# Kernel optimization log

Hardware: AMD Instinct MI355X
Metric: run time of the kernel (lower is better)

Reference implementation:

```python
import jax, jax.numpy as jnp
import numpy as np

B, L, T = 8, 4096, 128
D_H, D_G, D_PROJ = 1024, 256, 256


def setup_inputs() -> dict:
    key = jax.random.key(0)
    k1, k2, k3, k4, k5 = jax.random.split(key, 5)
    H = jax.random.normal(k1, (B, L, D_H), dtype=jnp.float32)
    G = jax.random.normal(k2, (B, T, D_G), dtype=jnp.float32)
    mask = jax.random.randint(k3, (B, L), 0, 2) == 1  # True = masked out
    Wk = jax.random.normal(k4, (D_H, D_PROJ), dtype=jnp.float32) * 0.02
    Wq = jax.random.normal(k5, (D_G, D_PROJ), dtype=jnp.float32) * 0.02
    return {"H": H, "G": G, "mask": mask, "Wk": Wk, "Wq": Wq}


def reference(H, G, mask, Wk, Wq):
    scale = D_PROJ ** (-0.5)
    K = jnp.einsum('bld,dp->blp', H, Wk)          # [B, L, d_proj]
    Q = jnp.einsum('btd,dp->btp', G, Wq)          # [B, T, d_proj]
    logits = jnp.einsum('btp,blp->btl', Q, K) * scale  # [B, T, L]
    logits = jnp.where(mask[:, None, :], -jnp.inf, logits)
    alpha = jax.nn.softmax(logits, axis=-1)       # [B, T, L]
    Z = jnp.einsum('btl,bld->btd', alpha, H)      # [B, T, d_h]
    return Z
```

## Files before the change

kernel.cpp:

```cpp
#include <hip/hip_runtime.h>
#include <hip/hip_bf16.h>
#include <math.h>

#define B_  8
#define L_  4096
#define T_  128
#define DH  1024
#define DG  256
#define DP  256
#define BK  64

typedef short bf16x8 __attribute__((ext_vector_type(8)));
typedef float f32x4  __attribute__((ext_vector_type(4)));

#define AS1(p) ((const __attribute__((address_space(1))) void*)(p))
#define AS3(p) ((__attribute__((address_space(3))) void*)(p))

__device__ __forceinline__ unsigned short f2bf(float f) {
    unsigned u = __float_as_uint(f);
    unsigned r = (u + 0x7FFFu + ((u >> 16) & 1u)) >> 16;
    return (unsigned short)r;
}

__global__ __launch_bounds__(256) void wct_kernel(const float* __restrict__ Wk,
                                                  const float* __restrict__ Wq,
                                                  unsigned short* __restrict__ Wct) {
    __shared__ __attribute__((aligned(16))) unsigned short As[128 * BK];
    __shared__ __attribute__((aligned(16))) unsigned short Bs[64 * BK];
    const int n0 = blockIdx.x * 64, m0 = blockIdx.y * 128;
    const int tid = threadIdx.x, wave = tid >> 6, lane = tid & 63;
    const int lm = lane & 15, quad = lane >> 4;
    const int wm = wave >> 1, wn = wave & 1;
    const int bc = (tid & 15) * 4, br = tid >> 4;
    f32x4 acc[4][2] = {};

    for (int k0 = 0; k0 < DP; k0 += BK) {
        #pragma unroll
        for (int s = 0; s < 8; ++s) {
            const int row = br + s * 16;
            const float4 v = *(const float4*)(Wk + (size_t)(m0 + row) * DP + k0 + bc);
            ushort4 p; p.x = f2bf(v.x); p.y = f2bf(v.y); p.z = f2bf(v.z); p.w = f2bf(v.w);
            *(ushort4*)(&As[row * BK + bc]) = p;
        }
        #pragma unroll
        for (int s = 0; s < 4; ++s) {
            const int row = br + s * 16;
            const float4 v = *(const float4*)(Wq + (size_t)(n0 + row) * DP + k0 + bc);
            ushort4 p; p.x = f2bf(v.x); p.y = f2bf(v.y); p.z = f2bf(v.z); p.w = f2bf(v.w);
            *(ushort4*)(&Bs[row * BK + bc]) = p;
        }
        __syncthreads();
        #pragma unroll
        for (int ks = 0; ks < 2; ++ks) {
            bf16x8 a[4], bf[2];
            #pragma unroll
            for (int i = 0; i < 4; ++i)
                a[i] = *(const bf16x8*)(&As[(wm * 64 + i * 16 + lm) * BK + ks * 32 + quad * 8]);
            #pragma unroll
            for (int j = 0; j < 2; ++j)
                bf[j] = *(const bf16x8*)(&Bs[(wn * 32 + j * 16 + lm) * BK + ks * 32 + quad * 8]);
            #pragma unroll
            for (int i = 0; i < 4; ++i)
                #pragma unroll
                for (int j = 0; j < 2; ++j)
                    acc[i][j] = __builtin_amdgcn_mfma_f32_16x16x32_bf16(a[i], bf[j], acc[i][j], 0, 0, 0);
        }
        __syncthreads();
    }
    unsigned short* Cb = Wct + (size_t)m0 * DG + n0;
    #pragma unroll
    for (int i = 0; i < 4; ++i)
        #pragma unroll
        for (int j = 0; j < 2; ++j)
            #pragma unroll
            for (int r = 0; r < 4; ++r)
                Cb[(size_t)(wm * 64 + i * 16 + quad * 4 + r) * DG + wn * 32 + j * 16 + lm] =
                    f2bf(acc[i][j][r] * 0.0625f);
}

__global__ __launch_bounds__(256) void qproj_kernel(const float* __restrict__ G,
                                                    const unsigned short* __restrict__ Wct,
                                                    unsigned short* __restrict__ Qk) {
    __shared__ __attribute__((aligned(16))) unsigned short As[128 * BK];
    __shared__ __attribute__((aligned(16))) unsigned short Bs[64 * BK];
    const int n0 = blockIdx.x * 64, m0 = blockIdx.y * 128;
    const int tid = threadIdx.x, wave = tid >> 6, lane = tid & 63;
    const int lm = lane & 15, quad = lane >> 4;
    const int wm = wave >> 1, wn = wave & 1;
    const int bc = (tid & 15) * 4, br = tid >> 4;
    const int ar = lane >> 3, akb = (lane & 7) * 8;
    f32x4 acc[4][2] = {};

    for (int k0 = 0; k0 < DG; k0 += BK) {
        #pragma unroll
        for (int s = 0; s < 8; ++s) {
            const int row = br + s * 16;
            const float4 v = *(const float4*)(G + (size_t)(m0 + row) * DG + k0 + bc);
            ushort4 p; p.x = f2bf(v.x); p.y = f2bf(v.y); p.z = f2bf(v.z); p.w = f2bf(v.w);
            *(ushort4*)(&As[row * BK + bc]) = p;
        }
        #pragma unroll
        for (int s = 0; s < 2; ++s) {
            const int rowb = s * 32 + wave * 8;
            const unsigned short* gp = Wct + (size_t)(n0 + rowb + ar) * DG + k0 + akb;
            __builtin_amdgcn_global_load_lds(AS1(gp), AS3(&Bs[rowb * BK]), 16, 0, 0);
        }
        __syncthreads();
        #pragma unroll
        for (int ks = 0; ks < 2; ++ks) {
            bf16x8 a[4], bf[2];
            #pragma unroll
            for (int i = 0; i < 4; ++i)
                a[i] = *(const bf16x8*)(&As[(wm * 64 + i * 16 + lm) * BK + ks * 32 + quad * 8]);
            #pragma unroll
            for (int j = 0; j < 2; ++j)
                bf[j] = *(const bf16x8*)(&Bs[(wn * 32 + j * 16 + lm) * BK + ks * 32 + quad * 8]);
            #pragma unroll
            for (int i = 0; i < 4; ++i)
                #pragma unroll
                for (int j = 0; j < 2; ++j)
                    acc[i][j] = __builtin_amdgcn_mfma_f32_16x16x32_bf16(a[i], bf[j], acc[i][j], 0, 0, 0);
        }
        __syncthreads();
    }
    unsigned short* Cb = Qk + (size_t)m0 * DH + n0;
    #pragma unroll
    for (int i = 0; i < 4; ++i)
        #pragma unroll
        for (int j = 0; j < 2; ++j)
            #pragma unroll
            for (int r = 0; r < 4; ++r)
                Cb[(size_t)(wm * 64 + i * 16 + quad * 4 + r) * DH + wn * 32 + j * 16 + lm] =
                    f2bf(acc[i][j][r]);
}

__global__ __launch_bounds__(256) void logits_kernel(const unsigned short* __restrict__ Qk,
                                                     const float* __restrict__ H,
                                                     float* __restrict__ logits) {
    __shared__ __attribute__((aligned(16))) unsigned short As[T_ * BK];
    __shared__ __attribute__((aligned(16))) unsigned short Bs[64 * BK];
    const int b = blockIdx.y, l0 = blockIdx.x * 64;
    const int tid = threadIdx.x, wave = tid >> 6, lane = tid & 63;
    const unsigned short* Ab = Qk + (size_t)b * T_ * DH;
    const float*          Hb = H + ((size_t)b * L_ + l0) * DH;

    const int lm = lane & 15, quad = lane >> 4;
    const int wm = wave >> 1, wn = wave & 1;
    f32x4 acc[4][2] = {};
    const int ar = lane >> 3, akb = (lane & 7) * 8;
    const int bc = (tid & 15) * 4, br0 = tid >> 4;

    for (int k0 = 0; k0 < DH; k0 += BK) {
        #pragma unroll
        for (int s = 0; s < 4; ++s) {
            const int rowb = s * 32 + wave * 8;
            const unsigned short* gp = Ab + (size_t)(rowb + ar) * DH + k0 + akb;
            __builtin_amdgcn_global_load_lds(AS1(gp), AS3(&As[rowb * BK]), 16, 0, 0);
        }
        #pragma unroll
        for (int s = 0; s < 4; ++s) {
            const int row = br0 + s * 16;
            const float4 v = *(const float4*)(Hb + (size_t)row * DH + k0 + bc);
            ushort4 p; p.x = f2bf(v.x); p.y = f2bf(v.y); p.z = f2bf(v.z); p.w = f2bf(v.w);
            *(ushort4*)(&Bs[row * BK + bc]) = p;
        }
        __syncthreads();
        #pragma unroll
        for (int ks = 0; ks < 2; ++ks) {
            bf16x8 a[4], bf[2];
            #pragma unroll
            for (int i = 0; i < 4; ++i)
                a[i] = *(const bf16x8*)(&As[(wm * 64 + i * 16 + lm) * BK + ks * 32 + quad * 8]);
            #pragma unroll
            for (int j = 0; j < 2; ++j)
                bf[j] = *(const bf16x8*)(&Bs[(wn * 32 + j * 16 + lm) * BK + ks * 32 + quad * 8]);
            #pragma unroll
            for (int i = 0; i < 4; ++i)
                #pragma unroll
                for (int j = 0; j < 2; ++j)
                    acc[i][j] = __builtin_amdgcn_mfma_f32_16x16x32_bf16(a[i], bf[j], acc[i][j], 0, 0, 0);
        }
        __syncthreads();
    }
    float* Cb = logits + (size_t)b * T_ * L_ + l0;
    #pragma unroll
    for (int i = 0; i < 4; ++i)
        #pragma unroll
        for (int j = 0; j < 2; ++j)
            #pragma unroll
            for (int r = 0; r < 4; ++r)
                Cb[(size_t)(wm * 64 + i * 16 + quad * 4 + r) * L_ + wn * 32 + j * 16 + lm] = acc[i][j][r];
}

__global__ __launch_bounds__(256) void softmax_kernel(const float* __restrict__ logits,
                                                      const int* __restrict__ mask,
                                                      unsigned short* __restrict__ alpha) {
    const int row = blockIdx.x;
    const int b   = row >> 7;
    const int tid = threadIdx.x;
    const float4* p4 = (const float4*)(logits + (size_t)row * L_);
    const int4*   m4 = (const int4*)(mask + (size_t)b * L_);

    float vals[4][4];
    float vmax = -3.0e38f;
    #pragma unroll
    for (int s = 0; s < 4; ++s) {
        const int idx = tid + s * 256;
        float4 v = p4[idx];
        const int4 mm = m4[idx];
        v.x = mm.x ? -3.0e38f : v.x;
        v.y = mm.y ? -3.0e38f : v.y;
        v.z = mm.z ? -3.0e38f : v.z;
        v.w = mm.w ? -3.0e38f : v.w;
        vals[s][0] = v.x; vals[s][1] = v.y; vals[s][2] = v.z; vals[s][3] = v.w;
        vmax = fmaxf(vmax, fmaxf(fmaxf(v.x, v.y), fmaxf(v.z, v.w)));
    }
    #pragma unroll
    for (int off = 32; off; off >>= 1) vmax = fmaxf(vmax, __shfl_down(vmax, off, 64));

    __shared__ float red[4];
    __shared__ float bcast;
    const int wid = tid >> 6, lane = tid & 63;
    if (lane == 0) red[wid] = vmax;
    __syncthreads();
    if (tid == 0) bcast = fmaxf(fmaxf(red[0], red[1]), fmaxf(red[2], red[3]));
    __syncthreads();
    const float m = bcast;

    float sum = 0.f;
    #pragma unroll
    for (int s = 0; s < 4; ++s)
        #pragma unroll
        for (int i = 0; i < 4; ++i) {
            vals[s][i] = __expf(vals[s][i] - m);
            sum += vals[s][i];
        }
    #pragma unroll
    for (int off = 32; off; off >>= 1) sum += __shfl_down(sum, off, 64);
    __syncthreads();
    if (lane == 0) red[wid] = sum;
    __syncthreads();
    if (tid == 0) bcast = red[0] + red[1] + red[2] + red[3];
    __syncthreads();
    const float inv = 1.0f / bcast;

    unsigned short* arow = alpha + (size_t)row * L_;
    #pragma unroll
    for (int s = 0; s < 4; ++s) {
        ushort4 p;
        p.x = f2bf(vals[s][0] * inv); p.y = f2bf(vals[s][1] * inv);
        p.z = f2bf(vals[s][2] * inv); p.w = f2bf(vals[s][3] * inv);
        *(ushort4*)(arow + (size_t)(tid + s * 256) * 4) = p;
    }
}

__global__ __launch_bounds__(256) void z_kernel(const unsigned short* __restrict__ alpha,
                                                const float* __restrict__ H,
                                                float* __restrict__ Z) {
    __shared__ __attribute__((aligned(16))) unsigned short As[T_ * BK];
    __shared__ __attribute__((aligned(16))) unsigned short Bs[64 * (BK + 2)];
    const int d0 = blockIdx.x * 64, b = blockIdx.y, ch = blockIdx.z;
    const int tid = threadIdx.x, wave = tid >> 6, lane = tid & 63;
    const int Lc = L_ / 4;
    const unsigned short* Ab = alpha + (size_t)b * T_ * L_ + ch * Lc;
    const float*          Hb = H + ((size_t)b * L_ + ch * Lc) * DH + d0;

    const int lm = lane & 15, quad = lane >> 4;
    const int wm = wave >> 1, wn = wave & 1;
    f32x4 acc[4][2] = {};
    const int ar = lane >> 3, akb = (lane & 7) * 8;
    const int dg = tid & 7, lp = tid >> 3;
    unsigned* B32 = (unsigned*)Bs;

    for (int k0 = 0; k0 < Lc; k0 += BK) {
        #pragma unroll
        for (int s = 0; s < 4; ++s) {
            const int rowb = s * 32 + wave * 8;
            const unsigned short* gp = Ab + (size_t)(rowb + ar) * L_ + k0 + akb;
            __builtin_amdgcn_global_load_lds(AS1(gp), AS3(&As[rowb * BK]), 16, 0, 0);
        }
        {
            const float* r0 = Hb + (size_t)(k0 + 2 * lp) * DH + dg * 8;
            const float4 v0a = *(const float4*)(r0);
            const float4 v0b = *(const float4*)(r0 + 4);
            const float4 v1a = *(const float4*)(r0 + DH);
            const float4 v1b = *(const float4*)(r0 + DH + 4);
            float a0[8] = {v0a.x, v0a.y, v0a.z, v0a.w, v0b.x, v0b.y, v0b.z, v0b.w};
            float a1[8] = {v1a.x, v1a.y, v1a.z, v1a.w, v1b.x, v1b.y, v1b.z, v1b.w};
            #pragma unroll
            for (int i = 0; i < 8; ++i) {
                const int d = dg * 8 + i;
                B32[d * 33 + lp] = (unsigned)f2bf(a0[i]) | ((unsigned)f2bf(a1[i]) << 16);
            }
        }
        __syncthreads();
        #pragma unroll
        for (int ks = 0; ks < 2; ++ks) {
            bf16x8 a[4], bf[2];
            #pragma unroll
            for (int i = 0; i < 4; ++i)
                a[i] = *(const bf16x8*)(&As[(wm * 64 + i * 16 + lm) * BK + ks * 32 + quad * 8]);
            #pragma unroll
            for (int j = 0; j < 2; ++j) {
                const int d = wn * 32 + j * 16 + lm;
                const unsigned* p = B32 + d * 33 + ks * 16 + quad * 4;
                union { bf16x8 v; unsigned u[4]; } f;
                f.u[0] = p[0]; f.u[1] = p[1]; f.u[2] = p[2]; f.u[3] = p[3];
                bf[j] = f.v;
            }
            #pragma unroll
            for (int i = 0; i < 4; ++i)
                #pragma unroll
                for (int j = 0; j < 2; ++j)
                    acc[i][j] = __builtin_amdgcn_mfma_f32_16x16x32_bf16(a[i], bf[j], acc[i][j], 0, 0, 0);
        }
        __syncthreads();
    }
    float* Cb = Z + (size_t)b * T_ * DH + d0;
    #pragma unroll
    for (int i = 0; i < 4; ++i)
        #pragma unroll
        for (int j = 0; j < 2; ++j)
            #pragma unroll
            for (int r = 0; r < 4; ++r)
                atomicAdd(&Cb[(size_t)(wm * 64 + i * 16 + quad * 4 + r) * DH + wn * 32 + j * 16 + lm],
                          acc[i][j][r]);
}

extern "C" void kernel_launch(void* const* d_in, const int* in_sizes, int n_in,
                              void* d_out, int out_size, void* d_ws, size_t ws_size,
                              hipStream_t stream) {
    const float* H    = (const float*)d_in[0];
    const float* G    = (const float*)d_in[1];
    const int*   mask = (const int*)d_in[2];
    const float* Wk   = (const float*)d_in[3];
    const float* Wq   = (const float*)d_in[4];
    float* Z = (float*)d_out;

    char* ws = (char*)d_ws;
    unsigned short* Wct    = (unsigned short*)ws;
    unsigned short* Qk     = (unsigned short*)(ws + ((size_t)1 << 20));
    float*          logits = (float*)(ws + ((size_t)4 << 20));
    unsigned short* alpha  = (unsigned short*)(ws + ((size_t)24 << 20));

    hipMemsetAsync(Z, 0, (size_t)out_size * sizeof(float), stream);
    wct_kernel<<<dim3(DG / 64, DH / 128), 256, 0, stream>>>(Wk, Wq, Wct);
    qproj_kernel<<<dim3(DH / 64, (B_ * T_) / 128), 256, 0, stream>>>(G, Wct, Qk);
    logits_kernel<<<dim3(L_ / 64, B_), 256, 0, stream>>>(Qk, H, logits);
    softmax_kernel<<<B_ * T_, 256, 0, stream>>>(logits, mask, alpha);
    z_kernel<<<dim3(DH / 64, B_, 4), 256, 0, stream>>>(alpha, H, Z);
}
```

Baseline: 285.4 us.

## Widen GEMM tiles to 128, split logits K into two partials, swizzle z LDS

The logits kernel now uses 128-wide L tiles and splits the D_H reduction into two halves. Each half writes a partial logits buffer, and softmax sums the two partials. The z kernel uses 128-wide D tiles, splits L into 8 chunks instead of 4, and adds an XOR-style rotation to the transposed LDS layout to avoid bank conflicts. Larger tiles reuse each Qk/alpha tile more per H load, at the cost of an extra partial logits buffer read/written, more atomics, and higher register pressure (launch_bounds 256,2).

After: 306.1 us. +7.3%, slower.

```diff
diff --git a/kernel.cpp b/kernel.cpp
--- a/kernel.cpp
+++ b/kernel.cpp
@@ -134,23 +134,23 @@
                     f2bf(acc[i][j][r]);
 }
 
-__global__ __launch_bounds__(256) void logits_kernel(const unsigned short* __restrict__ Qk,
-                                                     const float* __restrict__ H,
-                                                     float* __restrict__ logits) {
+__global__ __launch_bounds__(256, 2) void logits_kernel(const unsigned short* __restrict__ Qk,
+                                                        const float* __restrict__ H,
+                                                        float* __restrict__ part) {
     __shared__ __attribute__((aligned(16))) unsigned short As[T_ * BK];
-    __shared__ __attribute__((aligned(16))) unsigned short Bs[64 * BK];
-    const int b = blockIdx.y, l0 = blockIdx.x * 64;
+    __shared__ __attribute__((aligned(16))) unsigned short Bs[128 * BK];
+    const int l0 = blockIdx.x * 128, b = blockIdx.y, h = blockIdx.z;
     const int tid = threadIdx.x, wave = tid >> 6, lane = tid & 63;
-    const unsigned short* Ab = Qk + (size_t)b * T_ * DH;
-    const float*          Hb = H + ((size_t)b * L_ + l0) * DH;
+    const unsigned short* Ab = Qk + (size_t)b * T_ * DH + h * 512;
+    const float*          Hb = H + ((size_t)b * L_ + l0) * DH + h * 512;
 
     const int lm = lane & 15, quad = lane >> 4;
     const int wm = wave >> 1, wn = wave & 1;
-    f32x4 acc[4][2] = {};
+    f32x4 acc[4][4] = {};
     const int ar = lane >> 3, akb = (lane & 7) * 8;
-    const int bc = (tid & 15) * 4, br0 = tid >> 4;
-
-    for (int k0 = 0; k0 < DH; k0 += BK) {
+    const int bc = (tid & 15) * 4, br = tid >> 4;
+
+    for (int k0 = 0; k0 < 512; k0 += BK) {
         #pragma unroll
         for (int s = 0; s < 4; ++s) {
             const int rowb = s * 32 + wave * 8;
@@ -158,8 +158,8 @@
             __builtin_amdgcn_global_load_lds(AS1(gp), AS3(&As[rowb * BK]), 16, 0, 0);
         }
         #pragma unroll
-        for (int s = 0; s < 4; ++s) {
-            const int row = br0 + s * 16;
+        for (int s = 0; s < 8; ++s) {
+            const int row = br + s * 16;
             const float4 v = *(const float4*)(Hb + (size_t)row * DH + k0 + bc);
             ushort4 p; p.x = f2bf(v.x); p.y = f2bf(v.y); p.z = f2bf(v.z); p.w = f2bf(v.w);
             *(ushort4*)(&Bs[row * BK + bc]) = p;
@@ -167,38 +167,39 @@
         __syncthreads();
         #pragma unroll
         for (int ks = 0; ks < 2; ++ks) {
-            bf16x8 a[4], bf[2];
+            bf16x8 a[4], bf[4];
             #pragma unroll
             for (int i = 0; i < 4; ++i)
                 a[i] = *(const bf16x8*)(&As[(wm * 64 + i * 16 + lm) * BK + ks * 32 + quad * 8]);
             #pragma unroll
-            for (int j = 0; j < 2; ++j)
-                bf[j] = *(const bf16x8*)(&Bs[(wn * 32 + j * 16 + lm) * BK + ks * 32 + quad * 8]);
-            #pragma unroll
-            for (int i = 0; i < 4; ++i)
-                #pragma unroll
-                for (int j = 0; j < 2; ++j)
+            for (int j = 0; j < 4; ++j)
+                bf[j] = *(const bf16x8*)(&Bs[(wn * 64 + j * 16 + lm) * BK + ks * 32 + quad * 8]);
+            #pragma unroll
+            for (int i = 0; i < 4; ++i)
+                #pragma unroll
+                for (int j = 0; j < 4; ++j)
                     acc[i][j] = __builtin_amdgcn_mfma_f32_16x16x32_bf16(a[i], bf[j], acc[i][j], 0, 0, 0);
         }
         __syncthreads();
     }
-    float* Cb = logits + (size_t)b * T_ * L_ + l0;
+    float* Cb = part + ((size_t)h * B_ + b) * T_ * L_ + l0;
     #pragma unroll
     for (int i = 0; i < 4; ++i)
         #pragma unroll
-        for (int j = 0; j < 2; ++j)
+        for (int j = 0; j < 4; ++j)
             #pragma unroll
             for (int r = 0; r < 4; ++r)
-                Cb[(size_t)(wm * 64 + i * 16 + quad * 4 + r) * L_ + wn * 32 + j * 16 + lm] = acc[i][j][r];
-}
-
-__global__ __launch_bounds__(256) void softmax_kernel(const float* __restrict__ logits,
+                Cb[(size_t)(wm * 64 + i * 16 + quad * 4 + r) * L_ + wn * 64 + j * 16 + lm] = acc[i][j][r];
+}
+
+__global__ __launch_bounds__(256) void softmax_kernel(const float* __restrict__ part,
                                                       const int* __restrict__ mask,
                                                       unsigned short* __restrict__ alpha) {
     const int row = blockIdx.x;
     const int b   = row >> 7;
     const int tid = threadIdx.x;
-    const float4* p4 = (const float4*)(logits + (size_t)row * L_);
+    const float4* p0 = (const float4*)(part + (size_t)row * L_);
+    const float4* p1 = (const float4*)(part + (size_t)B_ * T_ * L_ + (size_t)row * L_);
     const int4*   m4 = (const int4*)(mask + (size_t)b * L_);
 
     float vals[4][4];
@@ -206,12 +207,13 @@
     #pragma unroll
     for (int s = 0; s < 4; ++s) {
         const int idx = tid + s * 256;
-        float4 v = p4[idx];
+        const float4 a = p0[idx], c = p1[idx];
         const int4 mm = m4[idx];
-        v.x = mm.x ? -3.0e38f : v.x;
-        v.y = mm.y ? -3.0e38f : v.y;
-        v.z = mm.z ? -3.0e38f : v.z;
-        v.w = mm.w ? -3.0e38f : v.w;
+        float4 v;
+        v.x = mm.x ? -3.0e38f : a.x + c.x;
+        v.y = mm.y ? -3.0e38f : a.y + c.y;
+        v.z = mm.z ? -3.0e38f : a.z + c.z;
+        v.w = mm.w ? -3.0e38f : a.w + c.w;
         vals[s][0] = v.x; vals[s][1] = v.y; vals[s][2] = v.z; vals[s][3] = v.w;
         vmax = fmaxf(vmax, fmaxf(fmaxf(v.x, v.y), fmaxf(v.z, v.w)));
     }
@@ -254,23 +256,22 @@
     }
 }
 
-__global__ __launch_bounds__(256) void z_kernel(const unsigned short* __restrict__ alpha,
-                                                const float* __restrict__ H,
-                                                float* __restrict__ Z) {
+__global__ __launch_bounds__(256, 2) void z_kernel(const unsigned short* __restrict__ alpha,
+                                                   const float* __restrict__ H,
+                                                   float* __restrict__ Z) {
     __shared__ __attribute__((aligned(16))) unsigned short As[T_ * BK];
-    __shared__ __attribute__((aligned(16))) unsigned short Bs[64 * (BK + 2)];
-    const int d0 = blockIdx.x * 64, b = blockIdx.y, ch = blockIdx.z;
+    __shared__ __attribute__((aligned(16))) unsigned B32[128 * 33];
+    const int d0 = blockIdx.x * 128, b = blockIdx.y, ch = blockIdx.z;
     const int tid = threadIdx.x, wave = tid >> 6, lane = tid & 63;
-    const int Lc = L_ / 4;
+    const int Lc = 512;
     const unsigned short* Ab = alpha + (size_t)b * T_ * L_ + ch * Lc;
     const float*          Hb = H + ((size_t)b * L_ + ch * Lc) * DH + d0;
 
     const int lm = lane & 15, quad = lane >> 4;
     const int wm = wave >> 1, wn = wave & 1;
-    f32x4 acc[4][2] = {};
+    f32x4 acc[4][4] = {};
     const int ar = lane >> 3, akb = (lane & 7) * 8;
-    const int dg = tid & 7, lp = tid >> 3;
-    unsigned* B32 = (unsigned*)Bs;
+    const int dg = tid & 15, lph = tid >> 4;
 
     for (int k0 = 0; k0 < Lc; k0 += BK) {
         #pragma unroll
@@ -279,8 +280,10 @@
             const unsigned short* gp = Ab + (size_t)(rowb + ar) * L_ + k0 + akb;
             __builtin_amdgcn_global_load_lds(AS1(gp), AS3(&As[rowb * BK]), 16, 0, 0);
         }
-        {
-            const float* r0 = Hb + (size_t)(k0 + 2 * lp) * DH + dg * 8;
+        #pragma unroll
+        for (int s = 0; s < 2; ++s) {
+            const int lpair = s * 16 + lph;
+            const float* r0 = Hb + (size_t)(k0 + 2 * lpair) * DH + dg * 8;
             const float4 v0a = *(const float4*)(r0);
             const float4 v0b = *(const float4*)(r0 + 4);
             const float4 v1a = *(const float4*)(r0 + DH);
@@ -290,28 +293,30 @@
             #pragma unroll
             for (int i = 0; i < 8; ++i) {
                 const int d = dg * 8 + i;
-                B32[d * 33 + lp] = (unsigned)f2bf(a0[i]) | ((unsigned)f2bf(a1[i]) << 16);
+                B32[d * 33 + ((lpair + (d >> 3)) & 31)] =
+                    (unsigned)f2bf(a0[i]) | ((unsigned)f2bf(a1[i]) << 16);
             }
         }
         __syncthreads();
         #pragma unroll
         for (int ks = 0; ks < 2; ++ks) {
-            bf16x8 a[4], bf[2];
+            bf16x8 a[4], bf[4];
             #pragma unroll
             for (int i = 0; i < 4; ++i)
                 a[i] = *(const bf16x8*)(&As[(wm * 64 + i * 16 + lm) * BK + ks * 32 + quad * 8]);
             #pragma unroll
-            for (int j = 0; j < 2; ++j) {
-                const int d = wn * 32 + j * 16 + lm;
-                const unsigned* p = B32 + d * 33 + ks * 16 + quad * 4;
+            for (int j = 0; j < 4; ++j) {
+                const int d = wn * 64 + j * 16 + lm;
                 union { bf16x8 v; unsigned u[4]; } f;
-                f.u[0] = p[0]; f.u[1] = p[1]; f.u[2] = p[2]; f.u[3] = p[3];
+                #pragma unroll
+                for (int i = 0; i < 4; ++i)
+                    f.u[i] = B32[d * 33 + ((ks * 16 + quad * 4 + i + (d >> 3)) & 31)];
                 bf[j] = f.v;
             }
             #pragma unroll
             for (int i = 0; i < 4; ++i)
                 #pragma unroll
-                for (int j = 0; j < 2; ++j)
+                for (int j = 0; j < 4; ++j)
                     acc[i][j] = __builtin_amdgcn_mfma_f32_16x16x32_bf16(a[i], bf[j], acc[i][j], 0, 0, 0);
         }
         __syncthreads();
@@ -320,10 +325,10 @@
     #pragma unroll
     for (int i = 0; i < 4; ++i)
         #pragma unroll
-        for (int j = 0; j < 2; ++j)
+        for (int j = 0; j < 4; ++j)
             #pragma unroll
             for (int r = 0; r < 4; ++r)
-                atomicAdd(&Cb[(size_t)(wm * 64 + i * 16 + quad * 4 + r) * DH + wn * 32 + j * 16 + lm],
+                atomicAdd(&Cb[(size_t)(wm * 64 + i * 16 + quad * 4 + r) * DH + wn * 64 + j * 16 + lm],
                           acc[i][j][r]);
 }
 
@@ -338,15 +343,15 @@
     float* Z = (float*)d_out;
 
     char* ws = (char*)d_ws;
-    unsigned short* Wct    = (unsigned short*)ws;
-    unsigned short* Qk     = (unsigned short*)(ws + ((size_t)1 << 20));
-    float*          logits = (float*)(ws + ((size_t)4 << 20));
-    unsigned short* alpha  = (unsigned short*)(ws + ((size_t)24 << 20));
+    unsigned short* Wct   = (unsigned short*)ws;
+    unsigned short* Qk    = (unsigned short*)(ws + ((size_t)1 << 20));
+    float*          part  = (float*)(ws + ((size_t)4 << 20));
+    unsigned short* alpha = (unsigned short*)(ws + ((size_t)40 << 20));
 
     hipMemsetAsync(Z, 0, (size_t)out_size * sizeof(float), stream);
     wct_kernel<<<dim3(DG / 64, DH / 128), 256, 0, stream>>>(Wk, Wq, Wct);
     qproj_kernel<<<dim3(DH / 64, (B_ * T_) / 128), 256, 0, stream>>>(G, Wct, Qk);
-    logits_kernel<<<dim3(L_ / 64, B_), 256, 0, stream>>>(Qk, H, logits);
-    softmax_kernel<<<B_ * T_, 256, 0, stream>>>(logits, mask, alpha);
-    z_kernel<<<dim3(DH / 64, B_, 4), 256, 0, stream>>>(alpha, H, Z);
-}
+    logits_kernel<<<dim3(L_ / 128, B_, 2), 256, 0, stream>>>(Qk, H, part);
+    softmax_kernel<<<B_ * T_, 256, 0, stream>>>(part, mask, alpha);
+    z_kernel<<<dim3(DH / 128, B_, 8), 256, 0, stream>>>(alpha, H, Z);
+}
```
